# Kernel optimization log

Hardware: AMD Instinct MI355X
Metric: run time of the kernel (lower is better)

The kernel has to match this reference:

```python
import jax, jax.numpy as jnp
import numpy as np

D_FEATURE = 1024
HEAD = 16
D_K = 64
D_V = 64
EPS = 1e-6


def setup_inputs() -> dict:
    key = jax.random.key(0)
    ks = jax.random.split(key, 12)
    B, S = 2, 2048
    s_in = 1.0 / np.sqrt(D_FEATURE)
    s_o = 1.0 / np.sqrt(HEAD * D_V)
    return {
        "q": jax.random.normal(ks[0], (B, S, D_FEATURE), jnp.float32),
        "k": jax.random.normal(ks[1], (B, S, D_FEATURE), jnp.float32),
        "v": jax.random.normal(ks[2], (B, S, D_FEATURE), jnp.float32),
        "Wq": jax.random.uniform(ks[3], (D_FEATURE, HEAD * D_K), jnp.float32, -s_in, s_in),
        "bq": jnp.zeros((HEAD * D_K,), jnp.float32),
        "Wk": jax.random.uniform(ks[4], (D_FEATURE, HEAD * D_K), jnp.float32, -s_in, s_in),
        "bk": jnp.zeros((HEAD * D_K,), jnp.float32),
        "Wv": jax.random.uniform(ks[5], (D_FEATURE, HEAD * D_V), jnp.float32, -s_in, s_in),
        "bv": jnp.zeros((HEAD * D_V,), jnp.float32),
        "Wo": jax.random.uniform(ks[6], (HEAD * D_V, D_FEATURE), jnp.float32, -s_o, s_o),
        "bo": jnp.zeros((D_FEATURE,), jnp.float32),
        "gamma": jnp.ones((D_FEATURE,), jnp.float32),
        "beta": jnp.zeros((D_FEATURE,), jnp.float32),
    }


def reference(q, k, v, Wq, bq, Wk, bk, Wv, bv, Wo, bo, gamma, beta):
    B, Sq, _ = q.shape
    Sk, Sv = k.shape[1], v.shape[1]
    shortcut = v
    # projections -> (b, h, s, d)
    qh = (q @ Wq + bq).reshape(B, Sq, HEAD, D_K).transpose(0, 2, 1, 3)
    kh = (k @ Wk + bk).reshape(B, Sk, HEAD, D_K).transpose(0, 2, 1, 3)
    vh = (v @ Wv + bv).reshape(B, Sv, HEAD, D_V).transpose(0, 2, 1, 3)
    scale = 1.0 / np.sqrt(D_K).astype(np.float32)
    scores = jnp.einsum('bhqd,bhkd->bhqk', qh * scale, kh)
    attn = jax.nn.softmax(scores, axis=-1)  # dropout is identity (p=0 / eval)
    ctx = jnp.einsum('bhqk,bhkd->bhqd', attn, vh)
    ctx = ctx.transpose(0, 2, 1, 3).reshape(B, Sv, HEAD * D_V)
    out = ctx @ Wo + bo
    out = out + shortcut
    # LayerNorm, eps=1e-6
    mu = out.mean(-1, keepdims=True)
    var = out.var(-1, keepdims=True)
    out = (out - mu) * jax.lax.rsqrt(var + EPS) * gamma + beta
    return out
```

## Files before the change

kernel.cpp:

```cpp
#include <hip/hip_runtime.h>

#define D_FEAT 1024
#define NTOK   4096
#define SEQ    2048
#define NHEAD  16
#define DK     64
#define QSCALE 0.1803368801111204f

typedef float          f32x4  __attribute__((ext_vector_type(4)));
typedef float          f32x16 __attribute__((ext_vector_type(16)));
typedef short          s16x8  __attribute__((ext_vector_type(8)));
typedef unsigned short u16x4  __attribute__((ext_vector_type(4)));

__device__ __forceinline__ unsigned short f2bf(float f) {
  union { float f; unsigned int u; } x; x.f = f;
  unsigned int r = x.u + 0x7fffu + ((x.u >> 16) & 1u);
  return (unsigned short)(r >> 16);
}
__device__ __forceinline__ unsigned short f2h(float f) {
  union { _Float16 h; unsigned short u; } x; x.h = (_Float16)f; return x.u;
}
__device__ __forceinline__ float h2f(unsigned short u) {
  union { _Float16 h; unsigned short u; } x; x.u = u; return (float)x.h;
}

__device__ __forceinline__ f32x4 mfma16(s16x8 a, s16x8 b, f32x4 c) {
  return __builtin_amdgcn_mfma_f32_16x16x32_bf16(a, b, c, 0, 0, 0);
}
__device__ __forceinline__ f32x16 mfma32(s16x8 a, s16x8 b, f32x16 c) {
  return __builtin_amdgcn_mfma_f32_32x32x16_bf16(a, b, c, 0, 0, 0);
}

__device__ __forceinline__ void gload16(const void* g, void* l) {
  __builtin_amdgcn_global_load_lds(
      (const __attribute__((address_space(1))) void*)g,
      (__attribute__((address_space(3))) void*)l, 16, 0, 0);
}

__global__ __launch_bounds__(256) void prep_kernel(
    const float* __restrict__ q, const float* __restrict__ k, const float* __restrict__ v,
    const float* __restrict__ Wq, const float* __restrict__ Wk,
    const float* __restrict__ Wv, const float* __restrict__ Wo,
    unsigned short* __restrict__ qb, unsigned short* __restrict__ kb,
    unsigned short* __restrict__ vb,
    unsigned short* __restrict__ WT, unsigned short* __restrict__ Wot)
{
  __shared__ float tile[32][33];
  const int bx = blockIdx.x, tid = threadIdx.x;
  if (bx < 12288) {
    int sel = bx >> 12;
    const float* src = sel == 0 ? q : (sel == 1 ? k : v);
    unsigned short* dst = sel == 0 ? qb : (sel == 1 ? kb : vb);
    size_t i = ((size_t)(bx & 4095) * 256 + tid) * 4;
    float4 f = *(const float4*)(src + i);
    u16x4 o; o.x = f2bf(f.x); o.y = f2bf(f.y); o.z = f2bf(f.z); o.w = f2bf(f.w);
    *(u16x4*)(dst + i) = o;
  } else {
    int t = bx - 12288;
    int z = t >> 10, rest = t & 1023;
    int bxt = rest & 31, byt = rest >> 5;
    const float* W = z == 0 ? Wq : z == 1 ? Wk : z == 2 ? Wv : Wo;
    unsigned short* T = (z < 3) ? (WT + (size_t)z * 1024 * 1024) : Wot;
    int tx = tid & 31, ty = tid >> 5;
    int n = bxt * 32 + tx;
    for (int i = 0; i < 4; ++i) {
      int kk = byt * 32 + ty + i * 8;
      tile[ty + i * 8][tx] = W[(size_t)kk * D_FEAT + n];
    }
    __syncthreads();
    int kk = byt * 32 + tx;
    for (int i = 0; i < 4; ++i) {
      int n2 = bxt * 32 + ty + i * 8;
      T[(size_t)n2 * D_FEAT + kk] = f2bf(tile[tx][ty + i * 8]);
    }
  }
}

__global__ __launch_bounds__(256, 3) void gemm_qkv(
    const unsigned short* __restrict__ qb, const unsigned short* __restrict__ kb,
    const unsigned short* __restrict__ vb, const unsigned short* __restrict__ WT,
    const float* __restrict__ bq, const float* __restrict__ bk, const float* __restrict__ bv,
    unsigned short* __restrict__ Qp, unsigned short* __restrict__ Kp, unsigned short* __restrict__ Vt)
{
  __shared__ __align__(16) unsigned short sAB[2 * 128 * 64];
  unsigned short* sA = sAB;
  unsigned short* sB = sAB + 128 * 64;
  const int tid = threadIdx.x;
  const int wave = tid >> 6, lane = tid & 63;
  const int quad = lane >> 4, l16 = lane & 15;
  const int wx = wave & 1, wy = wave >> 1;
  const int bx = blockIdx.x;
  const int chunk = bx >> 3;

  const unsigned short* rA;
  const unsigned short* rB;
  int m0, n0;
  if (chunk < 2) {
    m0 = blockIdx.y * 128; n0 = (bx & 7) * 128;
    rA = (chunk ? kb : qb) + (size_t)m0 * D_FEAT;
    rB = WT + (size_t)(chunk * 1024 + n0) * D_FEAT;
  } else {
    m0 = (bx & 7) * 128; n0 = blockIdx.y * 128;
    rA = WT + (size_t)(2048 + m0) * D_FEAT;
    rB = vb + (size_t)n0 * D_FEAT;
  }

  f32x4 acc[4][4];
  for (int mt = 0; mt < 4; ++mt)
    for (int nt = 0; nt < 4; ++nt) acc[mt][nt] = (f32x4){0.f, 0.f, 0.f, 0.f};

  const int rw8 = lane >> 3;
  const int cls = ((lane & 7) ^ (lane >> 3)) * 8;
  const int sw = l16 & 7;

  for (int k0 = 0; k0 < D_FEAT; k0 += 64) {
    __syncthreads();
    for (int j = 0; j < 4; ++j) {
      int ch = wave * 4 + j;
      gload16(rA + (size_t)(ch * 8 + rw8) * D_FEAT + k0 + cls, sA + ch * 512);
      gload16(rB + (size_t)(ch * 8 + rw8) * D_FEAT + k0 + cls, sB + ch * 512);
    }
    __syncthreads();
    s16x8 af[2][4], bfr[2][4];
    for (int kk = 0; kk < 2; ++kk) {
      int c = ((kk * 4 + quad) ^ sw) * 8;
      for (int mt = 0; mt < 4; ++mt)
        af[kk][mt] = *(const s16x8*)(sA + (wy * 64 + mt * 16 + l16) * 64 + c);
      for (int nt = 0; nt < 4; ++nt)
        bfr[kk][nt] = *(const s16x8*)(sB + (wx * 64 + nt * 16 + l16) * 64 + c);
    }
    for (int kk = 0; kk < 2; ++kk)
      for (int mt = 0; mt < 4; ++mt)
        for (int nt = 0; nt < 4; ++nt)
          acc[mt][nt] = mfma16(af[kk][mt], bfr[kk][nt], acc[mt][nt]);
  }

  if (chunk < 2) {
    const float* bias = chunk ? bk : bq;
    unsigned short* Cp = chunk ? Kp : Qp;
    const float scale = chunk == 0 ? QSCALE : 1.0f;
    for (int mt = 0; mt < 4; ++mt)
      for (int nt = 0; nt < 4; ++nt) {
        int col = n0 + wx * 64 + nt * 16 + l16;
        float bcol = bias[col];
        for (int r = 0; r < 4; ++r) {
          int row = m0 + wy * 64 + mt * 16 + quad * 4 + r;
          Cp[(size_t)row * D_FEAT + col] = f2bf((acc[mt][nt][r] + bcol) * scale);
        }
      }
  } else {
    for (int mt = 0; mt < 4; ++mt)
      for (int r = 0; r < 4; ++r) {
        float bfeat = bv[m0 + wy * 64 + mt * 16 + quad * 4 + r];
        for (int nt = 0; nt < 4; ++nt) acc[mt][nt][r] += bfeat;
      }
    unsigned short* tb = sAB;
    for (int p = 0; p < 2; ++p) {
      __syncthreads();
      if (wx == p) {
        for (int mt = 0; mt < 4; ++mt)
          for (int nt = 0; nt < 4; ++nt) {
            int tok_loc = nt * 16 + l16;
            for (int r = 0; r < 4; ++r) {
              int f_loc = wy * 64 + mt * 16 + quad * 4 + r;
              tb[f_loc * 72 + tok_loc] = f2bf(acc[mt][nt][r]);
            }
          }
      }
      __syncthreads();
      int n_base = n0 + p * 64;
      int b = n_base >> 11, tok0 = n_base & 2047;
      int ck = lane & 7;
      for (int j = 0; j < 4; ++j) {
        int f_loc = (wave * 4 + j) * 8 + rw8;
        int f = m0 + f_loc, hh = f >> 6, dv = f & 63;
        *(s16x8*)(Vt + ((size_t)(b * 16 + hh) * 64 + dv) * SEQ + tok0 + ck * 8) =
            *(const s16x8*)(tb + f_loc * 72 + ck * 8);
      }
    }
  }
}

__global__ __launch_bounds__(256) void gemm_o(
    const unsigned short* __restrict__ A, const unsigned short* __restrict__ Bt,
    const float* __restrict__ bias, const float* __restrict__ resid,
    float* __restrict__ Cout)
{
  __shared__ __align__(16) unsigned short sA[128 * 64];
  __shared__ __align__(16) unsigned short sB[64 * 64];
  const int tid = threadIdx.x;
  const int wave = tid >> 6, lane = tid & 63;
  const int quad = lane >> 4, l16 = lane & 15;
  const int wx = wave & 1, wy = wave >> 1;
  const int n0 = blockIdx.x * 64, m0 = blockIdx.y * 128;

  f32x4 acc[4][2];
  for (int mt = 0; mt < 4; ++mt)
    for (int nt = 0; nt < 2; ++nt) acc[mt][nt] = (f32x4){0.f, 0.f, 0.f, 0.f};

  const int rw8 = lane >> 3;
  const int cls = ((lane & 7) ^ (lane >> 3)) * 8;
  const int sw = l16 & 7;

  for (int k0 = 0; k0 < D_FEAT; k0 += 64) {
    __syncthreads();
    for (int j = 0; j < 4; ++j) {
      int ch = wave * 4 + j;
      gload16(A + (size_t)(m0 + ch * 8 + rw8) * D_FEAT + k0 + cls, sA + ch * 512);
    }
    for (int j = 0; j < 2; ++j) {
      int ch = wave * 2 + j;
      gload16(Bt + (size_t)(n0 + ch * 8 + rw8) * D_FEAT + k0 + cls, sB + ch * 512);
    }
    __syncthreads();
    s16x8 af[2][4], bfr[2][2];
    for (int kk = 0; kk < 2; ++kk) {
      int c = ((kk * 4 + quad) ^ sw) * 8;
      for (int mt = 0; mt < 4; ++mt)
        af[kk][mt] = *(const s16x8*)(sA + (wy * 64 + mt * 16 + l16) * 64 + c);
      for (int nt = 0; nt < 2; ++nt)
        bfr[kk][nt] = *(const s16x8*)(sB + (wx * 32 + nt * 16 + l16) * 64 + c);
    }
    for (int kk = 0; kk < 2; ++kk)
      for (int mt = 0; mt < 4; ++mt)
        for (int nt = 0; nt < 2; ++nt)
          acc[mt][nt] = mfma16(af[kk][mt], bfr[kk][nt], acc[mt][nt]);
  }

  for (int mt = 0; mt < 4; ++mt)
    for (int nt = 0; nt < 2; ++nt) {
      int col = n0 + wx * 32 + nt * 16 + l16;
      float bcol = bias[col];
      for (int r = 0; r < 4; ++r) {
        int row = m0 + wy * 64 + mt * 16 + quad * 4 + r;
        Cout[(size_t)row * D_FEAT + col] =
            acc[mt][nt][r] + bcol + resid[(size_t)row * D_FEAT + col];
      }
    }
}

__global__ __launch_bounds__(256, 4) void flash_part(
    const unsigned short* __restrict__ Qp,
    const unsigned short* __restrict__ Kp,
    const unsigned short* __restrict__ Vt,
    unsigned short* __restrict__ Opart,
    float* __restrict__ L)
{
  __shared__ __align__(16) unsigned short sQ[128 * 64];
  __shared__ __align__(16) unsigned short sK[64 * 64];
  __shared__ __align__(16) unsigned short sV[64 * 64];

  const int tid = threadIdx.x;
  const int wave = tid >> 6, lane = tid & 63;
  const int l32 = lane & 31, h = lane >> 5;

  const int blk = blockIdx.x;
  const int xcd = blk & 7, jj = blk >> 3;
  const int grp = xcd * 8 + (jj >> 4);
  const int q0 = (jj & 15) * 128;
  const int bh = grp & 31, z = grp >> 5;
  const int b = bh >> 4, hd = bh & 15;
  const int kbase = z * (SEQ / 2);
  const size_t base = (size_t)b * SEQ * D_FEAT + (size_t)hd * DK;
  const unsigned short* vt = Vt + (size_t)bh * 64 * SEQ;

  const int rw8 = lane >> 3;
  const int cls = ((lane & 7) ^ (lane >> 3)) * 8;

  for (int j = 0; j < 4; ++j) {
    int ch = wave * 4 + j;
    gload16(Qp + base + (size_t)(q0 + ch * 8 + rw8) * D_FEAT + cls, sQ + ch * 512);
  }
  __syncthreads();

  const int qrow = wave * 32 + l32;
  const int qsw = qrow & 7;
  s16x8 bq[4];
  for (int s = 0; s < 4; ++s)
    bq[s] = *(const s16x8*)(sQ + qrow * 64 + ((2 * s + h) ^ qsw) * 8);

  unsigned short* sP = sQ;

  f32x16 o0, o1;
  for (int r = 0; r < 16; ++r) { o0[r] = 0.f; o1[r] = 0.f; }
  float lsum = 0.f;

  const int ksw0 = l32 & 7;

  for (int k0 = kbase; k0 < kbase + SEQ / 2; k0 += 64) {
    __syncthreads();
    for (int j = 0; j < 2; ++j) {
      int ch = wave * 2 + j;
      gload16(Kp + base + (size_t)(k0 + ch * 8 + rw8) * D_FEAT + cls, sK + ch * 512);
      gload16(vt + (size_t)(ch * 8 + rw8) * SEQ + k0 + cls, sV + ch * 512);
    }
    __syncthreads();

    f32x16 st0, st1;
    for (int r = 0; r < 16; ++r) { st0[r] = 0.f; st1[r] = 0.f; }
    for (int s = 0; s < 4; ++s) {
      int csw = ((2 * s + h) ^ ksw0) * 8;
      s16x8 a0 = *(const s16x8*)(sK + l32 * 64 + csw);
      s16x8 a1 = *(const s16x8*)(sK + (32 + l32) * 64 + csw);
      st0 = mfma32(a0, bq[s], st0);
      st1 = mfma32(a1, bq[s], st1);
    }

    const int rowb = qrow * 64;
    for (int g = 0; g < 4; ++g) {
      unsigned int u[4];
      for (int r = 0; r < 4; ++r) {
        union { float f; unsigned int v; } x;
        x.f = __builtin_exp2f(st0[4 * g + r]);
        lsum += x.f; u[r] = x.v;
      }
      unsigned int w0 = __builtin_amdgcn_perm(u[1], u[0], 0x07060302u);
      unsigned int w1 = __builtin_amdgcn_perm(u[3], u[2], 0x07060302u);
      *(uint2*)(sP + rowb + ((g ^ qsw) * 8) + 4 * h) = make_uint2(w0, w1);
    }
    for (int g = 0; g < 4; ++g) {
      unsigned int u[4];
      for (int r = 0; r < 4; ++r) {
        union { float f; unsigned int v; } x;
        x.f = __builtin_exp2f(st1[4 * g + r]);
        lsum += x.f; u[r] = x.v;
      }
      unsigned int w0 = __builtin_amdgcn_perm(u[1], u[0], 0x07060302u);
      unsigned int w1 = __builtin_amdgcn_perm(u[3], u[2], 0x07060302u);
      *(uint2*)(sP + rowb + (((4 + g) ^ qsw) * 8) + 4 * h) = make_uint2(w0, w1);
    }

    s16x8 bp[4];
    for (int s = 0; s < 4; ++s)
      bp[s] = *(const s16x8*)(sP + rowb + ((2 * s + h) ^ qsw) * 8);

    for (int s = 0; s < 4; ++s) {
      int csw = ((2 * s + h) ^ ksw0) * 8;
      s16x8 a0 = *(const s16x8*)(sV + l32 * 64 + csw);
      s16x8 a1 = *(const s16x8*)(sV + (32 + l32) * 64 + csw);
      o0 = mfma32(a0, bp[s], o0);
      o1 = mfma32(a1, bp[s], o1);
    }
  }

  lsum += __shfl_xor(lsum, 32, 64);
  const size_t trow = (size_t)(z * 32 + bh) * SEQ + (q0 + qrow);
  unsigned short* orow = Opart + trow * 64;
  for (int g = 0; g < 4; ++g) {
    u16x4 ov;
    for (int r = 0; r < 4; ++r) ov[r] = f2h(o0[4 * g + r]);
    *(u16x4*)(orow + 8 * g + 4 * h) = ov;
  }
  for (int g = 0; g < 4; ++g) {
    u16x4 ov;
    for (int r = 0; r < 4; ++r) ov[r] = f2h(o1[4 * g + r]);
    *(u16x4*)(orow + 32 + 8 * g + 4 * h) = ov;
  }
  if (h == 0) L[trow] = lsum;
}

__global__ __launch_bounds__(256) void combine_kernel(
    const unsigned short* __restrict__ Opart, const float* __restrict__ L,
    unsigned short* __restrict__ ctx)
{
  const int idx = blockIdx.x * 256 + threadIdx.x;
  const int dq = idx & 15;
  const int trow = idx >> 4;
  const int bh = trow >> 11, tok = trow & 2047;
  const int b = bh >> 4, h = bh & 15;
  const int HS = 32 * SEQ;

  float inv = __builtin_amdgcn_rcpf(L[trow] + L[HS + trow]);

  u16x4 p0 = *(const u16x4*)(Opart + (size_t)trow * 64 + dq * 4);
  u16x4 p1 = *(const u16x4*)(Opart + ((size_t)HS + trow) * 64 + dq * 4);
  u16x4 o;
  for (int r = 0; r < 4; ++r)
    o[r] = f2bf((h2f(p0[r]) + h2f(p1[r])) * inv);
  *(u16x4*)(ctx + (size_t)b * SEQ * D_FEAT + (size_t)tok * D_FEAT + h * 64 + dq * 4) = o;
}

__global__ __launch_bounds__(256) void ln_kernel(
    const float* __restrict__ x, const float* __restrict__ gamma,
    const float* __restrict__ beta, float* __restrict__ out)
{
  const int row = blockIdx.x, tid = threadIdx.x;
  const int wave = tid >> 6, lane = tid & 63;
  const float* xr = x + (size_t)row * D_FEAT;
  float4 v = ((const float4*)xr)[tid];
  float s  = v.x + v.y + v.z + v.w;
  float ss = v.x * v.x + v.y * v.y + v.z * v.z + v.w * v.w;
  for (int off = 1; off < 64; off <<= 1) {
    s  += __shfl_xor(s,  off, 64);
    ss += __shfl_xor(ss, off, 64);
  }
  __shared__ float red[8];
  if (lane == 0) { red[wave] = s; red[wave + 4] = ss; }
  __syncthreads();
  s  = red[0] + red[1] + red[2] + red[3];
  ss = red[4] + red[5] + red[6] + red[7];
  float mean = s * (1.f / D_FEAT);
  float var  = ss * (1.f / D_FEAT) - mean * mean;
  float rstd = rsqrtf(var + 1e-6f);
  float4 g  = ((const float4*)gamma)[tid];
  float4 bt = ((const float4*)beta)[tid];
  float4 o;
  o.x = (v.x - mean) * rstd * g.x + bt.x;
  o.y = (v.y - mean) * rstd * g.y + bt.y;
  o.z = (v.z - mean) * rstd * g.z + bt.z;
  o.w = (v.w - mean) * rstd * g.w + bt.w;
  ((float4*)(out + (size_t)row * D_FEAT))[tid] = o;
}

extern "C" void kernel_launch(void* const* d_in, const int* in_sizes, int n_in,
                              void* d_out, int out_size, void* d_ws, size_t ws_size,
                              hipStream_t stream) {
  const float* q     = (const float*)d_in[0];
  const float* k     = (const float*)d_in[1];
  const float* v     = (const float*)d_in[2];
  const float* Wq    = (const float*)d_in[3];
  const float* bq    = (const float*)d_in[4];
  const float* Wk    = (const float*)d_in[5];
  const float* bk    = (const float*)d_in[6];
  const float* Wv    = (const float*)d_in[7];
  const float* bv    = (const float*)d_in[8];
  const float* Wo    = (const float*)d_in[9];
  const float* bo    = (const float*)d_in[10];
  const float* gamma = (const float*)d_in[11];
  const float* beta  = (const float*)d_in[12];

  char* w = (char*)d_ws;
  const size_t MB = 1u << 20;
  unsigned short* qb    = (unsigned short*)(w + 0 * MB);
  unsigned short* kb    = (unsigned short*)(w + 8 * MB);
  unsigned short* vb    = (unsigned short*)(w + 16 * MB);
  unsigned short* WT    = (unsigned short*)(w + 24 * MB);
  unsigned short* Wot   = (unsigned short*)(w + 30 * MB);
  unsigned short* Qp    = (unsigned short*)(w + 32 * MB);
  unsigned short* Kp    = (unsigned short*)(w + 40 * MB);
  unsigned short* Vt    = (unsigned short*)(w + 48 * MB);
  unsigned short* ctx   = (unsigned short*)(w + 56 * MB);
  float*          tmp   = (float*)(w + 64 * MB);
  unsigned short* Opart = (unsigned short*)(w + 0 * MB);
  float*          L     = (float*)(w + 16 * MB);

  prep_kernel<<<16384, 256, 0, stream>>>(q, k, v, Wq, Wk, Wv, Wo, qb, kb, vb, WT, Wot);

  gemm_qkv<<<dim3(24, 32), 256, 0, stream>>>(qb, kb, vb, WT, bq, bk, bv, Qp, Kp, Vt);

  flash_part<<<1024, 256, 0, stream>>>(Qp, Kp, Vt, Opart, L);

  combine_kernel<<<4096, 256, 0, stream>>>(Opart, L, ctx);

  gemm_o<<<dim3(16, 32), 256, 0, stream>>>(ctx, Wot, bo, v, tmp);

  ln_kernel<<<NTOK, 256, 0, stream>>>(tmp, gamma, beta, (float*)d_out);
}
```

Measured before the change: 241.7 us.

## Split flash attention keys four ways and combine four partial planes

Raises the flash-attention split-K factor from 2 to 4, doubling the grid to 2048 blocks, each handling a quarter of the key range. The partial outputs are spread over three planes in the low workspace plus one plane reused from the later tmp region, and the combine kernel now sums four partials and four L values. Occupancy hint rises to 5 blocks per CU. The aim is better CU utilisation and latency hiding, paid for with more partial-output traffic and redundant Q loads.

```diff
diff --git a/kernel.cpp b/kernel.cpp
--- a/kernel.cpp
+++ b/kernel.cpp
@@ -6,6 +6,7 @@
 #define NHEAD  16
 #define DK     64
 #define QSCALE 0.1803368801111204f
+#define PLANE  (32 * SEQ * 64)
 
 typedef float          f32x4  __attribute__((ext_vector_type(4)));
 typedef float          f32x16 __attribute__((ext_vector_type(16)));
@@ -239,11 +240,12 @@
     }
 }
 
-__global__ __launch_bounds__(256, 4) void flash_part(
+__global__ __launch_bounds__(256, 5) void flash_part(
     const unsigned short* __restrict__ Qp,
     const unsigned short* __restrict__ Kp,
     const unsigned short* __restrict__ Vt,
-    unsigned short* __restrict__ Opart,
+    unsigned short* __restrict__ OpLo,
+    unsigned short* __restrict__ Op3,
     float* __restrict__ L)
 {
   __shared__ __align__(16) unsigned short sQ[128 * 64];
@@ -256,11 +258,11 @@
 
   const int blk = blockIdx.x;
   const int xcd = blk & 7, jj = blk >> 3;
-  const int grp = xcd * 8 + (jj >> 4);
+  const int grp = xcd * 16 + (jj >> 4);
   const int q0 = (jj & 15) * 128;
   const int bh = grp & 31, z = grp >> 5;
   const int b = bh >> 4, hd = bh & 15;
-  const int kbase = z * (SEQ / 2);
+  const int kbase = z * (SEQ / 4);
   const size_t base = (size_t)b * SEQ * D_FEAT + (size_t)hd * DK;
   const unsigned short* vt = Vt + (size_t)bh * 64 * SEQ;
 
@@ -287,7 +289,7 @@
 
   const int ksw0 = l32 & 7;
 
-  for (int k0 = kbase; k0 < kbase + SEQ / 2; k0 += 64) {
+  for (int k0 = kbase; k0 < kbase + SEQ / 4; k0 += 64) {
     __syncthreads();
     for (int j = 0; j < 2; ++j) {
       int ch = wave * 2 + j;
@@ -344,8 +346,9 @@
   }
 
   lsum += __shfl_xor(lsum, 32, 64);
-  const size_t trow = (size_t)(z * 32 + bh) * SEQ + (q0 + qrow);
-  unsigned short* orow = Opart + trow * 64;
+  const int trow0 = bh * SEQ + (q0 + qrow);
+  unsigned short* plane = (z < 3) ? (OpLo + (size_t)z * PLANE) : Op3;
+  unsigned short* orow = plane + (size_t)trow0 * 64;
   for (int g = 0; g < 4; ++g) {
     u16x4 ov;
     for (int r = 0; r < 4; ++r) ov[r] = f2h(o0[4 * g + r]);
@@ -356,27 +359,31 @@
     for (int r = 0; r < 4; ++r) ov[r] = f2h(o1[4 * g + r]);
     *(u16x4*)(orow + 32 + 8 * g + 4 * h) = ov;
   }
-  if (h == 0) L[trow] = lsum;
+  if (h == 0) L[z * (32 * SEQ) + trow0] = lsum;
 }
 
 __global__ __launch_bounds__(256) void combine_kernel(
-    const unsigned short* __restrict__ Opart, const float* __restrict__ L,
-    unsigned short* __restrict__ ctx)
+    const unsigned short* __restrict__ OpLo, const unsigned short* __restrict__ Op3,
+    const float* __restrict__ L, unsigned short* __restrict__ ctx)
 {
   const int idx = blockIdx.x * 256 + threadIdx.x;
   const int dq = idx & 15;
-  const int trow = idx >> 4;
-  const int bh = trow >> 11, tok = trow & 2047;
+  const int trow0 = idx >> 4;
+  const int bh = trow0 >> 11, tok = trow0 & 2047;
   const int b = bh >> 4, h = bh & 15;
-  const int HS = 32 * SEQ;
-
-  float inv = __builtin_amdgcn_rcpf(L[trow] + L[HS + trow]);
-
-  u16x4 p0 = *(const u16x4*)(Opart + (size_t)trow * 64 + dq * 4);
-  u16x4 p1 = *(const u16x4*)(Opart + ((size_t)HS + trow) * 64 + dq * 4);
+
+  float lsum = L[trow0] + L[32 * SEQ + trow0] + L[2 * 32 * SEQ + trow0] +
+               L[3 * 32 * SEQ + trow0];
+  float inv = __builtin_amdgcn_rcpf(lsum);
+
+  float acc[4] = {0.f, 0.f, 0.f, 0.f};
+  for (int p = 0; p < 4; ++p) {
+    const unsigned short* plane = (p < 3) ? (OpLo + (size_t)p * PLANE) : Op3;
+    u16x4 pv = *(const u16x4*)(plane + (size_t)trow0 * 64 + dq * 4);
+    for (int r = 0; r < 4; ++r) acc[r] += h2f(pv[r]);
+  }
   u16x4 o;
-  for (int r = 0; r < 4; ++r)
-    o[r] = f2bf((h2f(p0[r]) + h2f(p1[r])) * inv);
+  for (int r = 0; r < 4; ++r) o[r] = f2bf(acc[r] * inv);
   *(u16x4*)(ctx + (size_t)b * SEQ * D_FEAT + (size_t)tok * D_FEAT + h * 64 + dq * 4) = o;
 }
 
@@ -441,16 +448,17 @@
   unsigned short* Vt    = (unsigned short*)(w + 48 * MB);
   unsigned short* ctx   = (unsigned short*)(w + 56 * MB);
   float*          tmp   = (float*)(w + 64 * MB);
-  unsigned short* Opart = (unsigned short*)(w + 0 * MB);
-  float*          L     = (float*)(w + 16 * MB);
+  unsigned short* OpLo  = (unsigned short*)(w + 0 * MB);
+  unsigned short* Op3   = (unsigned short*)(w + 64 * MB);
+  float*          L     = (float*)(w + 24 * MB);
 
   prep_kernel<<<16384, 256, 0, stream>>>(q, k, v, Wq, Wk, Wv, Wo, qb, kb, vb, WT, Wot);
 
   gemm_qkv<<<dim3(24, 32), 256, 0, stream>>>(qb, kb, vb, WT, bq, bk, bv, Qp, Kp, Vt);
 
-  flash_part<<<1024, 256, 0, stream>>>(Qp, Kp, Vt, Opart, L);
-
-  combine_kernel<<<4096, 256, 0, stream>>>(Opart, L, ctx);
+  flash_part<<<2048, 256, 0, stream>>>(Qp, Kp, Vt, OpLo, Op3, L);
+
+  combine_kernel<<<4096, 256, 0, stream>>>(OpLo, Op3, L, ctx);
 
   gemm_o<<<dim3(16, 32), 256, 0, stream>>>(ctx, Wot, bo, v, tmp);
 
```

Measured after the change: 351.3 us. +45.3%, slower.
